# Performance work log

Measured on AMD Instinct MI355X. Metric: run time of the kernel, lower is better.

## Reference

```python
import jax, jax.numpy as jnp
import numpy as np
import math

B, T, C, H = 2, 2048, 1024, 16
HD = C // H
WINDOW = 256  # local_attn_ctx with attnblocksize=1


def setup_inputs() -> dict:
    key = jax.random.key(0)
    k1, k2, k3 = jax.random.split(key, 3)
    x = jax.random.normal(k1, (B, T, C), dtype=jnp.float32)
    Wqkv = jax.random.normal(k2, (C, 3 * C), dtype=jnp.float32) * 0.02
    bqkv = jnp.zeros((3 * C,), dtype=jnp.float32)
    Wproj = jax.random.normal(k3, (C, C), dtype=jnp.float32) * 0.02
    bproj = jnp.zeros((C,), dtype=jnp.float32)
    # 'local' block-sparse layout at token granularity: causal + sliding window
    i = np.arange(T)[:, None]
    j = np.arange(T)[None, :]
    mask = ((j <= i) & (i - j <= WINDOW)).astype(np.int32)
    return {"x": x, "Wqkv": Wqkv, "bqkv": bqkv, "Wproj": Wproj, "bproj": bproj,
            "mask": jnp.asarray(mask)}


def reference(x, Wqkv, bqkv, Wproj, bproj, mask):
    Bb, Tt, Cc = x.shape
    qkv = (x @ Wqkv + bqkv).reshape(Bb, Tt, 3, H, HD)  # [B,T,3,H,hd]
    q = jnp.transpose(qkv[:, :, 0], (0, 2, 1, 3))  # [B,H,T,hd]
    k = jnp.transpose(qkv[:, :, 1], (0, 2, 1, 3))
    v = jnp.transpose(qkv[:, :, 2], (0, 2, 1, 3))
    scale = 1.0 / math.sqrt(HD)
    att = jnp.einsum('bhqd,bhkd->bhqk', q, k) * scale  # dense T x T scores
    att = jnp.where(mask[:Tt, :Tt] == 0, -jnp.inf, att)
    att = jax.nn.softmax(att, axis=-1)
    y = jnp.einsum('bhqk,bhkd->bhqd', att, v)
    y = jnp.transpose(y, (0, 2, 1, 3)).reshape(Bb, Tt, Cc)
    return y @ Wproj + bproj
```

## Files before the change

### kernel.cpp

```cpp
#include <hip/hip_runtime.h>
#include <hip/hip_bf16.h>
#include <math.h>

typedef __bf16 bf16;
typedef __attribute__((ext_vector_type(8))) __bf16 bf16x8;
typedef __attribute__((ext_vector_type(4))) __bf16 bf16x4;
typedef __attribute__((ext_vector_type(4))) float f32x4;

#define B_  2
#define T_  2048
#define C_  1024
#define H_  16
#define HD_ 64
#define WIN_ 256

#define GLOAD16(g, l)                                                        \
  __builtin_amdgcn_global_load_lds(                                          \
      (const __attribute__((address_space(1))) void*)(g),                    \
      (__attribute__((address_space(3))) void*)(l), 16, 0, 0)

__device__ inline void bar() {
  asm volatile("" ::: "memory");
  __builtin_amdgcn_s_barrier();
  asm volatile("" ::: "memory");
}


__global__ __launch_bounds__(256) void prologue_k(const float* __restrict__ x,
                                                  bf16* __restrict__ xb,
                                                  const float* __restrict__ Wqkv,
                                                  bf16* __restrict__ wqkvT,
                                                  const float* __restrict__ Wproj,
                                                  bf16* __restrict__ wprojT) {
  __shared__ float t[32][33];
  const int blk = blockIdx.x;
  const int tid = threadIdx.x;

  if (blk < 4096) {
    const int idx = blk * 256 + tid;
    const float4 v = ((const float4*)x)[idx];
    bf16x4 o;
    o[0] = (bf16)v.x; o[1] = (bf16)v.y; o[2] = (bf16)v.z; o[3] = (bf16)v.w;
    ((bf16x4*)xb)[idx] = o;
    return;
  }

  const float* W; bf16* WT; int N, tb;
  if (blk < 4096 + 3072) { tb = blk - 4096; W = Wqkv;  WT = wqkvT;  N = 3 * C_; }
  else                   { tb = blk - 7168; W = Wproj; WT = wprojT; N = C_;     }
  const int xt = N / 32;
  const int n0 = (tb % xt) * 32, k0 = (tb / xt) * 32;
  const int tx = tid & 31, ty = tid >> 5;

  #pragma unroll
  for (int i = 0; i < 32; i += 8)
    t[ty + i][tx] = W[(size_t)(k0 + ty + i) * N + (n0 + tx)];
  __syncthreads();
  #pragma unroll
  for (int i = 0; i < 32; i += 8)
    WT[(size_t)(n0 + ty + i) * C_ + (k0 + tx)] = (bf16)t[tx][ty + i];
}


template <int TM, int TN, int WM, int WN, int MINW, int MODE>
__global__ __launch_bounds__(WM * WN * 64, MINW)
void gemm_db_k(const bf16* __restrict__ A, const bf16* __restrict__ Bt,
               const float* __restrict__ bias,
               void* __restrict__ out0, void* __restrict__ out1,
               int M, int N, int K) {
  constexpr int NW    = WM * WN;
  constexpr int WROWS = TM / WM;
  constexpr int WCOLS = TN / WN;
  constexpr int FM    = WROWS / 16;
  constexpr int FN    = WCOLS / 16;
  constexpr int NCH   = (TM + TN) / 8;
  constexpr int CPW   = NCH / NW;

  const int bm = blockIdx.x * TM;
  const int bn = blockIdx.y * TN;
  const int tid  = threadIdx.x;
  const int wid  = tid >> 6;
  const int lane = tid & 63;
  const int wr = wid / WN;
  const int wc = wid % WN;
  const int lr = lane & 15;
  const int g  = lane >> 4;

  __shared__ bf16 As[2][TM * 64];
  __shared__ bf16 Bs[2][TN * 64];

  f32x4 acc[FM][FN] = {};

  const int sr = lane >> 3;
  const int sc = ((lane & 7) ^ sr) << 3;

  #define STG(p_, u_)                                                        \
    do {                                                                     \
      _Pragma("unroll")                                                      \
      for (int i = 0; i < CPW; ++i) {                                        \
        const int c = wid * CPW + i;                                         \
        if (c < TM / 8) {                                                    \
          GLOAD16(A + (size_t)(bm + c * 8 + sr) * K + (u_) * 64 + sc,        \
                  &As[p_][c * 8 * 64]);                                      \
        } else {                                                             \
          GLOAD16(Bt + (size_t)(bn + (c - TM / 8) * 8 + sr) * K + (u_) * 64 + sc, \
                  &Bs[p_][(c - TM / 8) * 8 * 64]);                           \
        }                                                                    \
      }                                                                      \
    } while (0)

  const int NT = K >> 6;
  const int kc0 = ((0 + g) ^ (lr & 7)) << 3;
  const int kc1 = ((4 + g) ^ (lr & 7)) << 3;

  STG(0, 0);
  asm volatile("s_waitcnt vmcnt(0)" ::: "memory");
  __builtin_amdgcn_s_barrier();
  asm volatile("" ::: "memory");

  for (int u = 0; u < NT; ++u) {
    const int p = u & 1;
    if (u + 1 < NT) {
      STG(p ^ 1, u + 1);
      asm volatile("s_waitcnt vmcnt(%0)" :: "i"(CPW) : "memory");
    } else {
      asm volatile("s_waitcnt vmcnt(0)" ::: "memory");
    }
    bar();

    const bf16* Ar = &As[p][(wr * WROWS + lr) * 64];
    const bf16* Br = &Bs[p][(wc * WCOLS + lr) * 64];
    #pragma unroll
    for (int s = 0; s < 2; ++s) {
      const int kc = s ? kc1 : kc0;
      bf16x8 av[FM], bvv[FN];
      #pragma unroll
      for (int m = 0; m < FM; ++m)
        av[m] = *(const bf16x8*)(Ar + m * 16 * 64 + kc);
      #pragma unroll
      for (int n = 0; n < FN; ++n)
        bvv[n] = *(const bf16x8*)(Br + n * 16 * 64 + kc);
      __builtin_amdgcn_s_setprio(1);
      #pragma unroll
      for (int m = 0; m < FM; ++m)
        #pragma unroll
        for (int n = 0; n < FN; ++n)
          acc[m][n] = __builtin_amdgcn_mfma_f32_16x16x32_bf16(av[m], bvv[n], acc[m][n], 0, 0, 0);
      __builtin_amdgcn_s_setprio(0);
    }
    bar();
  }
  #undef STG

  const int orow = g * 4;
  #pragma unroll
  for (int n = 0; n < FN; ++n) {
    const int nbase = bn + wc * WCOLS + n * 16;
    const int gn = nbase + lr;
    const float bv_ = bias[gn];
    #pragma unroll
    for (int m = 0; m < FM; ++m) {
      const int gm0 = bm + wr * WROWS + m * 16 + orow;
      if (MODE == 0) {
        #pragma unroll
        for (int r = 0; r < 4; ++r)
          ((float*)out0)[(size_t)(gm0 + r) * N + gn] = acc[m][n][r] + bv_;
      } else {
        if (nbase < 2 * C_) {
          #pragma unroll
          for (int r = 0; r < 4; ++r)
            ((bf16*)out0)[(size_t)(gm0 + r) * (2 * C_) + gn] = (bf16)(acc[m][n][r] + bv_);
        } else {
          const int vcol = gn - 2 * C_;
          const int h = vcol >> 6, d = vcol & 63;
          const int b = gm0 >> 11, tok = gm0 & (T_ - 1);
          bf16x4 o;
          #pragma unroll
          for (int r = 0; r < 4; ++r) o[r] = (bf16)(acc[m][n][r] + bv_);
          *(bf16x4*)&((bf16*)out1)[(((size_t)b * H_ + h) * HD_ + d) * T_ + tok] = o;
        }
      }
    }
  }
}


__global__ __launch_bounds__(512) void attn_mfma2_k(const bf16* __restrict__ qk,
                                                    const bf16* __restrict__ vt,
                                                    bf16* __restrict__ y) {
  const int q0 = blockIdx.x * 128;
  const int h  = blockIdx.y;
  const int b  = blockIdx.z;
  const int tid  = threadIdx.x;
  const int wid  = tid >> 6;
  const int lane = tid & 63;
  const int lr = lane & 15;
  const int g  = lane >> 4;

  __shared__ bf16 Ks[2][64 * 64];
  __shared__ bf16 Vs[2][64 * 64];
  __shared__ bf16 Ps[8][16][72];

  const int qrow = q0 + wid * 16 + lr;
  const bf16* qptr = qk + ((size_t)(b * T_ + qrow)) * (2 * C_) + h * HD_;
  bf16x8 qf0 = *(const bf16x8*)(qptr + g * 8);
  bf16x8 qf1 = *(const bf16x8*)(qptr + 32 + g * 8);

  float m = -1e30f, l = 0.f;
  f32x4 yacc[4] = {};

  const int bx = blockIdx.x;
  const int kt_lo = (bx * 2 >= 4) ? bx * 2 - 4 : 0;
  const int kt_hi = bx * 2 + 1;

  const int sr = lane >> 3;
  const int sc = ((lane & 7) ^ sr) << 3;
  const int kc0 = ((0 + g) ^ (lr & 7)) << 3;
  const int kc1 = ((4 + g) ^ (lr & 7)) << 3;

  #define STAGEKV(p_, kt_)                                                     \
    do {                                                                       \
      _Pragma("unroll")                                                        \
      for (int i = 0; i < 2; ++i) {                                            \
        const int c = wid * 2 + i;                                             \
        if (c < 8)                                                             \
          GLOAD16(qk + ((size_t)(b * T_) + (kt_) * 64 + c * 8 + sr) * (2 * C_) \
                       + C_ + h * HD_ + sc,                                    \
                  &Ks[p_][c * 8 * 64]);                                        \
        else                                                                   \
          GLOAD16(vt + (((size_t)b * H_ + h) * HD_ + (c - 8) * 8 + sr) * T_    \
                       + (kt_) * 64 + sc,                                      \
                  &Vs[p_][(c - 8) * 8 * 64]);                                  \
      }                                                                        \
    } while (0)

  STAGEKV(0, kt_lo);
  asm volatile("s_waitcnt vmcnt(0)" ::: "memory");
  bar();

  for (int kt = kt_lo; kt <= kt_hi; ++kt) {
    const int idx = kt - kt_lo;
    const int p   = idx & 1;
    if (kt + 1 <= kt_hi) {
      STAGEKV(p ^ 1, kt + 1);
      asm volatile("s_waitcnt vmcnt(2)" ::: "memory");
    } else {
      asm volatile("s_waitcnt vmcnt(0)" ::: "memory");
    }
    bar();

    const int wq = q0 + wid * 16;
    if (kt * 64 <= wq + 15 && kt * 64 + 63 >= wq - WIN_) {
      f32x4 sacc[4] = {};
      __builtin_amdgcn_s_setprio(1);
      #pragma unroll
      for (int t = 0; t < 4; ++t) {
        sacc[t] = __builtin_amdgcn_mfma_f32_16x16x32_bf16(
            *(const bf16x8*)&Ks[p][(t * 16 + lr) * 64 + kc0], qf0, sacc[t], 0, 0, 0);
        sacc[t] = __builtin_amdgcn_mfma_f32_16x16x32_bf16(
            *(const bf16x8*)&Ks[p][(t * 16 + lr) * 64 + kc1], qf1, sacc[t], 0, 0, 0);
      }
      __builtin_amdgcn_s_setprio(0);

      float pv[4][4];
      float rmax = -1e30f;
      #pragma unroll
      for (int t = 0; t < 4; ++t)
        #pragma unroll
        for (int r = 0; r < 4; ++r) {
          const int key = kt * 64 + t * 16 + g * 4 + r;
          const bool valid = (key <= qrow) && (qrow - key <= WIN_);
          const float sv = valid ? sacc[t][r] * 0.125f : -__builtin_inff();
          pv[t][r] = sv;
          rmax = fmaxf(rmax, sv);
        }
      rmax = fmaxf(rmax, __shfl_xor(rmax, 16));
      rmax = fmaxf(rmax, __shfl_xor(rmax, 32));

      const float mnew = fmaxf(m, rmax);
      const float alpha = __expf(m - mnew);
      m = mnew;
      float lsum = 0.f;
      #pragma unroll
      for (int t = 0; t < 4; ++t)
        #pragma unroll
        for (int r = 0; r < 4; ++r) {
          const float e = __expf(pv[t][r] - mnew);
          pv[t][r] = e;
          lsum += e;
        }
      lsum += __shfl_xor(lsum, 16);
      lsum += __shfl_xor(lsum, 32);
      l = l * alpha + lsum;

      #pragma unroll
      for (int t = 0; t < 4; ++t) {
        bf16x4 pk;
        #pragma unroll
        for (int r = 0; r < 4; ++r) pk[r] = (bf16)pv[t][r];
        *(bf16x4*)&Ps[wid][lr][t * 16 + g * 4] = pk;
      }

      float al[4];
      #pragma unroll
      for (int r = 0; r < 4; ++r) al[r] = __shfl(alpha, g * 4 + r);
      #pragma unroll
      for (int t = 0; t < 4; ++t)
        #pragma unroll
        for (int r = 0; r < 4; ++r) yacc[t][r] *= al[r];

      bf16x8 pf0 = *(const bf16x8*)&Ps[wid][lr][g * 8];
      bf16x8 pf1 = *(const bf16x8*)&Ps[wid][lr][32 + g * 8];
      __builtin_amdgcn_s_setprio(1);
      #pragma unroll
      for (int t = 0; t < 4; ++t) {
        yacc[t] = __builtin_amdgcn_mfma_f32_16x16x32_bf16(
            pf0, *(const bf16x8*)&Vs[p][(t * 16 + lr) * 64 + kc0], yacc[t], 0, 0, 0);
        yacc[t] = __builtin_amdgcn_mfma_f32_16x16x32_bf16(
            pf1, *(const bf16x8*)&Vs[p][(t * 16 + lr) * 64 + kc1], yacc[t], 0, 0, 0);
      }
      __builtin_amdgcn_s_setprio(0);
    }
    bar();
  }
  #undef STAGEKV

  float li[4];
  #pragma unroll
  for (int r = 0; r < 4; ++r) li[r] = 1.f / __shfl(l, g * 4 + r);
  #pragma unroll
  for (int t = 0; t < 4; ++t)
    #pragma unroll
    for (int r = 0; r < 4; ++r) {
      const int tok = q0 + wid * 16 + g * 4 + r;
      y[((size_t)(b * T_ + tok)) * C_ + h * HD_ + t * 16 + lr] = (bf16)(yacc[t][r] * li[r]);
    }
}


extern "C" void kernel_launch(void* const* d_in, const int* in_sizes, int n_in,
                              void* d_out, int out_size, void* d_ws, size_t ws_size,
                              hipStream_t stream) {
  const float* x     = (const float*)d_in[0];
  const float* Wqkv  = (const float*)d_in[1];
  const float* bqkv  = (const float*)d_in[2];
  const float* Wproj = (const float*)d_in[3];
  const float* bproj = (const float*)d_in[4];
  float* out = (float*)d_out;

  const size_t SZ_QK  = (size_t)B_ * T_ * 2 * C_ * sizeof(bf16);
  const size_t SZ_VT  = (size_t)B_ * H_ * HD_ * T_ * sizeof(bf16);
  const size_t SZ_XB  = (size_t)B_ * T_ * C_ * sizeof(bf16);
  const size_t SZ_WQT = (size_t)3 * C_ * C_ * sizeof(bf16);
  const size_t SZ_WPT = (size_t)C_ * C_ * sizeof(bf16);
  const size_t NEED   = SZ_QK + SZ_VT + SZ_XB + SZ_WQT + SZ_WPT + SZ_XB;
  if (ws_size < NEED) return;

  char* ws = (char*)d_ws;
  bf16* qkb    = (bf16*)(ws);
  bf16* vtb    = (bf16*)(ws + SZ_QK);
  bf16* xb     = (bf16*)(ws + SZ_QK + SZ_VT);
  bf16* wqkvT  = (bf16*)(ws + SZ_QK + SZ_VT + SZ_XB);
  bf16* wprojT = (bf16*)(ws + SZ_QK + SZ_VT + SZ_XB + SZ_WQT);
  bf16* yb     = (bf16*)(ws + SZ_QK + SZ_VT + SZ_XB + SZ_WQT + SZ_WPT);

  prologue_k<<<8192, 256, 0, stream>>>(x, xb, Wqkv, wqkvT, Wproj, wprojT);

  gemm_db_k<64, 96, 2, 2, 4, 2><<<dim3((B_ * T_) / 64, (3 * C_) / 96), 256, 0, stream>>>(
      xb, wqkvT, bqkv, qkb, vtb, B_ * T_, 3 * C_, C_);

  attn_mfma2_k<<<dim3(T_ / 128, H_, B_), 512, 0, stream>>>(qkb, vtb, yb);

  gemm_db_k<64, 128, 2, 2, 2, 0><<<dim3((B_ * T_) / 64, C_ / 128), 256, 0, stream>>>(
      yb, wprojT, bproj, out, nullptr, B_ * T_, C_, C_);
}
```

Baseline: 89.22 us.

## Fuse all stages into one cooperative persistent kernel with grid syncs

Replaces the four separate launches (prologue, QKV GEMM, attention, projection GEMM) with a single cooperative kernel of 512 blocks of 512 threads. A grid-wide sync separates the phases, and shared memory is reused from one pool. The QKV GEMM tile grows to 128x192 with 8 warps, the prologue is re-mapped to 512 blocks, and there is a multi-launch fallback if the cooperative launch fails. This removes launch gaps and tail effects between kernels, at the cost of grid-sync overhead, occupancy limits from a 80KB LDS pool, and fewer blocks per phase.

```diff
diff --git a/kernel.cpp b/kernel.cpp
--- a/kernel.cpp
+++ b/kernel.cpp
@@ -1,6 +1,9 @@
 #include <hip/hip_runtime.h>
+#include <hip/hip_cooperative_groups.h>
 #include <hip/hip_bf16.h>
 #include <math.h>
+
+namespace cg = cooperative_groups;
 
 typedef __bf16 bf16;
 typedef __attribute__((ext_vector_type(8))) __bf16 bf16x8;
@@ -26,48 +29,52 @@
 }
 
 
-__global__ __launch_bounds__(256) void prologue_k(const float* __restrict__ x,
-                                                  bf16* __restrict__ xb,
-                                                  const float* __restrict__ Wqkv,
-                                                  bf16* __restrict__ wqkvT,
-                                                  const float* __restrict__ Wproj,
-                                                  bf16* __restrict__ wprojT) {
-  __shared__ float t[32][33];
-  const int blk = blockIdx.x;
+__device__ __forceinline__ void prologue_phase(const float* __restrict__ x,
+                                               bf16* __restrict__ xb,
+                                               const float* __restrict__ Wqkv,
+                                               bf16* __restrict__ wqkvT,
+                                               const float* __restrict__ Wproj,
+                                               bf16* __restrict__ wprojT,
+                                               float* tf, int bid) {
   const int tid = threadIdx.x;
-
-  if (blk < 4096) {
-    const int idx = blk * 256 + tid;
+  #pragma unroll
+  for (int i = 0; i < 4; ++i) {
+    const int idx = (bid * 512 + tid) + i * 262144;
     const float4 v = ((const float4*)x)[idx];
     bf16x4 o;
     o[0] = (bf16)v.x; o[1] = (bf16)v.y; o[2] = (bf16)v.z; o[3] = (bf16)v.w;
     ((bf16x4*)xb)[idx] = o;
-    return;
-  }
-
-  const float* W; bf16* WT; int N, tb;
-  if (blk < 4096 + 3072) { tb = blk - 4096; W = Wqkv;  WT = wqkvT;  N = 3 * C_; }
-  else                   { tb = blk - 7168; W = Wproj; WT = wprojT; N = C_;     }
-  const int xt = N / 32;
-  const int n0 = (tb % xt) * 32, k0 = (tb / xt) * 32;
-  const int tx = tid & 31, ty = tid >> 5;
-
-  #pragma unroll
-  for (int i = 0; i < 32; i += 8)
-    t[ty + i][tx] = W[(size_t)(k0 + ty + i) * N + (n0 + tx)];
-  __syncthreads();
-  #pragma unroll
-  for (int i = 0; i < 32; i += 8)
-    WT[(size_t)(n0 + ty + i) * C_ + (k0 + tx)] = (bf16)t[tx][ty + i];
-}
-
-
-template <int TM, int TN, int WM, int WN, int MINW, int MODE>
-__global__ __launch_bounds__(WM * WN * 64, MINW)
-void gemm_db_k(const bf16* __restrict__ A, const bf16* __restrict__ Bt,
-               const float* __restrict__ bias,
-               void* __restrict__ out0, void* __restrict__ out1,
-               int M, int N, int K) {
+  }
+  const int half = tid >> 8;
+  const int st = tid & 255;
+  const int tx = st & 31, ty = st >> 5;
+  float* tt = tf + half * (32 * 33);
+  for (int j = 0; j < 4; ++j) {
+    const int tile = bid * 8 + j * 2 + half;
+    const float* W; bf16* WT; int N, tb;
+    if (tile < 3072) { tb = tile;        W = Wqkv;  WT = wqkvT;  N = 3 * C_; }
+    else             { tb = tile - 3072; W = Wproj; WT = wprojT; N = C_;     }
+    const int xt = N / 32;
+    const int n0 = (tb % xt) * 32, k0 = (tb / xt) * 32;
+    #pragma unroll
+    for (int i = 0; i < 32; i += 8)
+      tt[(ty + i) * 33 + tx] = W[(size_t)(k0 + ty + i) * N + (n0 + tx)];
+    __syncthreads();
+    #pragma unroll
+    for (int i = 0; i < 32; i += 8)
+      WT[(size_t)(n0 + ty + i) * C_ + (k0 + tx)] = (bf16)tt[tx * 33 + (ty + i)];
+    __syncthreads();
+  }
+}
+
+template <int TM, int TN, int WM, int WN, int MODE>
+__device__ __forceinline__ void gemm_phase(const bf16* __restrict__ A,
+                                           const bf16* __restrict__ Bt,
+                                           const float* __restrict__ bias,
+                                           void* __restrict__ out0,
+                                           void* __restrict__ out1,
+                                           int M, int N, int K,
+                                           bf16* pool, int bx, int by) {
   constexpr int NW    = WM * WN;
   constexpr int WROWS = TM / WM;
   constexpr int WCOLS = TN / WN;
@@ -76,8 +83,11 @@
   constexpr int NCH   = (TM + TN) / 8;
   constexpr int CPW   = NCH / NW;
 
-  const int bm = blockIdx.x * TM;
-  const int bn = blockIdx.y * TN;
+  bf16* As = pool;
+  bf16* Bs = pool + 2 * TM * 64;
+
+  const int bm = bx * TM;
+  const int bn = by * TN;
   const int tid  = threadIdx.x;
   const int wid  = tid >> 6;
   const int lane = tid & 63;
@@ -86,25 +96,22 @@
   const int lr = lane & 15;
   const int g  = lane >> 4;
 
-  __shared__ bf16 As[2][TM * 64];
-  __shared__ bf16 Bs[2][TN * 64];
-
   f32x4 acc[FM][FN] = {};
 
   const int sr = lane >> 3;
   const int sc = ((lane & 7) ^ sr) << 3;
 
-  #define STG(p_, u_)                                                        \
+  #define STGF(p_, u_)                                                       \
     do {                                                                     \
       _Pragma("unroll")                                                      \
       for (int i = 0; i < CPW; ++i) {                                        \
         const int c = wid * CPW + i;                                         \
         if (c < TM / 8) {                                                    \
           GLOAD16(A + (size_t)(bm + c * 8 + sr) * K + (u_) * 64 + sc,        \
-                  &As[p_][c * 8 * 64]);                                      \
+                  As + (p_) * TM * 64 + c * 8 * 64);                         \
         } else {                                                             \
           GLOAD16(Bt + (size_t)(bn + (c - TM / 8) * 8 + sr) * K + (u_) * 64 + sc, \
-                  &Bs[p_][(c - TM / 8) * 8 * 64]);                           \
+                  Bs + (p_) * TN * 64 + (c - TM / 8) * 8 * 64);              \
         }                                                                    \
       }                                                                      \
     } while (0)
@@ -113,7 +120,7 @@
   const int kc0 = ((0 + g) ^ (lr & 7)) << 3;
   const int kc1 = ((4 + g) ^ (lr & 7)) << 3;
 
-  STG(0, 0);
+  STGF(0, 0);
   asm volatile("s_waitcnt vmcnt(0)" ::: "memory");
   __builtin_amdgcn_s_barrier();
   asm volatile("" ::: "memory");
@@ -121,15 +128,15 @@
   for (int u = 0; u < NT; ++u) {
     const int p = u & 1;
     if (u + 1 < NT) {
-      STG(p ^ 1, u + 1);
+      STGF(p ^ 1, u + 1);
       asm volatile("s_waitcnt vmcnt(%0)" :: "i"(CPW) : "memory");
     } else {
       asm volatile("s_waitcnt vmcnt(0)" ::: "memory");
     }
     bar();
 
-    const bf16* Ar = &As[p][(wr * WROWS + lr) * 64];
-    const bf16* Br = &Bs[p][(wc * WCOLS + lr) * 64];
+    const bf16* Ar = As + p * TM * 64 + (wr * WROWS + lr) * 64;
+    const bf16* Br = Bs + p * TN * 64 + (wc * WCOLS + lr) * 64;
     #pragma unroll
     for (int s = 0; s < 2; ++s) {
       const int kc = s ? kc1 : kc0;
@@ -150,7 +157,7 @@
     }
     bar();
   }
-  #undef STG
+  #undef STGF
 
   const int orow = g * 4;
   #pragma unroll
@@ -184,23 +191,21 @@
   }
 }
 
-
-__global__ __launch_bounds__(512) void attn_mfma2_k(const bf16* __restrict__ qk,
-                                                    const bf16* __restrict__ vt,
-                                                    bf16* __restrict__ y) {
-  const int q0 = blockIdx.x * 128;
-  const int h  = blockIdx.y;
-  const int b  = blockIdx.z;
+__device__ __forceinline__ void attn_phase(const bf16* __restrict__ qk,
+                                           const bf16* __restrict__ vt,
+                                           bf16* __restrict__ y,
+                                           bf16* pool, int bx, int h, int b) {
+  bf16* Ks = pool;
+  bf16* Vs = pool + 8192;
+  bf16* Ps = pool + 16384;
+
+  const int q0 = bx * 128;
   const int tid  = threadIdx.x;
   const int wid  = tid >> 6;
   const int lane = tid & 63;
   const int lr = lane & 15;
   const int g  = lane >> 4;
 
-  __shared__ bf16 Ks[2][64 * 64];
-  __shared__ bf16 Vs[2][64 * 64];
-  __shared__ bf16 Ps[8][16][72];
-
   const int qrow = q0 + wid * 16 + lr;
   const bf16* qptr = qk + ((size_t)(b * T_ + qrow)) * (2 * C_) + h * HD_;
   bf16x8 qf0 = *(const bf16x8*)(qptr + g * 8);
@@ -209,7 +214,6 @@
   float m = -1e30f, l = 0.f;
   f32x4 yacc[4] = {};
 
-  const int bx = blockIdx.x;
   const int kt_lo = (bx * 2 >= 4) ? bx * 2 - 4 : 0;
   const int kt_hi = bx * 2 + 1;
 
@@ -226,11 +230,11 @@
         if (c < 8)                                                             \
           GLOAD16(qk + ((size_t)(b * T_) + (kt_) * 64 + c * 8 + sr) * (2 * C_) \
                        + C_ + h * HD_ + sc,                                    \
-                  &Ks[p_][c * 8 * 64]);                                        \
+                  Ks + (p_) * 4096 + c * 8 * 64);                              \
         else                                                                   \
           GLOAD16(vt + (((size_t)b * H_ + h) * HD_ + (c - 8) * 8 + sr) * T_    \
                        + (kt_) * 64 + sc,                                      \
-                  &Vs[p_][(c - 8) * 8 * 64]);                                  \
+                  Vs + (p_) * 4096 + (c - 8) * 8 * 64);                        \
       }                                                                        \
     } while (0)
 
@@ -256,9 +260,9 @@
       #pragma unroll
       for (int t = 0; t < 4; ++t) {
         sacc[t] = __builtin_amdgcn_mfma_f32_16x16x32_bf16(
-            *(const bf16x8*)&Ks[p][(t * 16 + lr) * 64 + kc0], qf0, sacc[t], 0, 0, 0);
+            *(const bf16x8*)(Ks + p * 4096 + (t * 16 + lr) * 64 + kc0), qf0, sacc[t], 0, 0, 0);
         sacc[t] = __builtin_amdgcn_mfma_f32_16x16x32_bf16(
-            *(const bf16x8*)&Ks[p][(t * 16 + lr) * 64 + kc1], qf1, sacc[t], 0, 0, 0);
+            *(const bf16x8*)(Ks + p * 4096 + (t * 16 + lr) * 64 + kc1), qf1, sacc[t], 0, 0, 0);
       }
       __builtin_amdgcn_s_setprio(0);
 
@@ -298,7 +302,7 @@
         bf16x4 pk;
         #pragma unroll
         for (int r = 0; r < 4; ++r) pk[r] = (bf16)pv[t][r];
-        *(bf16x4*)&Ps[wid][lr][t * 16 + g * 4] = pk;
+        *(bf16x4*)(Ps + (wid * 16 + lr) * 72 + t * 16 + g * 4) = pk;
       }
 
       float al[4];
@@ -309,15 +313,15 @@
         #pragma unroll
         for (int r = 0; r < 4; ++r) yacc[t][r] *= al[r];
 
-      bf16x8 pf0 = *(const bf16x8*)&Ps[wid][lr][g * 8];
-      bf16x8 pf1 = *(const bf16x8*)&Ps[wid][lr][32 + g * 8];
+      bf16x8 pf0 = *(const bf16x8*)(Ps + (wid * 16 + lr) * 72 + g * 8);
+      bf16x8 pf1 = *(const bf16x8*)(Ps + (wid * 16 + lr) * 72 + 32 + g * 8);
       __builtin_amdgcn_s_setprio(1);
       #pragma unroll
       for (int t = 0; t < 4; ++t) {
         yacc[t] = __builtin_amdgcn_mfma_f32_16x16x32_bf16(
-            pf0, *(const bf16x8*)&Vs[p][(t * 16 + lr) * 64 + kc0], yacc[t], 0, 0, 0);
+            pf0, *(const bf16x8*)(Vs + p * 4096 + (t * 16 + lr) * 64 + kc0), yacc[t], 0, 0, 0);
         yacc[t] = __builtin_amdgcn_mfma_f32_16x16x32_bf16(
-            pf1, *(const bf16x8*)&Vs[p][(t * 16 + lr) * 64 + kc1], yacc[t], 0, 0, 0);
+            pf1, *(const bf16x8*)(Vs + p * 4096 + (t * 16 + lr) * 64 + kc1), yacc[t], 0, 0, 0);
       }
       __builtin_amdgcn_s_setprio(0);
     }
@@ -338,6 +342,55 @@
 }
 
 
+__global__ __launch_bounds__(512, 4) void fused_k(
+    const float* __restrict__ x, bf16* __restrict__ xb,
+    const float* __restrict__ Wqkv, bf16* __restrict__ wqkvT,
+    const float* __restrict__ Wproj, bf16* __restrict__ wprojT,
+    const float* __restrict__ bqkv, const float* __restrict__ bproj,
+    bf16* __restrict__ qkb, bf16* __restrict__ vtb,
+    bf16* __restrict__ yb, float* __restrict__ out) {
+  __shared__ __align__(16) bf16 pool[40960];
+  cg::grid_group grid = cg::this_grid();
+  const int bid = blockIdx.x;
+
+  prologue_phase(x, xb, Wqkv, wqkvT, Wproj, wprojT, (float*)pool, bid);
+  grid.sync();
+  gemm_phase<128, 192, 2, 4, 2>(xb, wqkvT, bqkv, qkb, vtb,
+                                B_ * T_, 3 * C_, C_, pool, bid & 31, bid >> 5);
+  grid.sync();
+  attn_phase(qkb, vtb, yb, pool, bid & 15, (bid >> 4) & 15, bid >> 8);
+  grid.sync();
+  gemm_phase<64, 128, 2, 4, 0>(yb, wprojT, bproj, out, nullptr,
+                               B_ * T_, C_, C_, pool, bid & 63, bid >> 6);
+}
+
+
+__global__ __launch_bounds__(512) void prologue_k(const float* x, bf16* xb,
+    const float* Wqkv, bf16* wqkvT, const float* Wproj, bf16* wprojT) {
+  __shared__ __align__(16) float tf[2 * 32 * 33];
+  prologue_phase(x, xb, Wqkv, wqkvT, Wproj, wprojT, tf, blockIdx.x);
+}
+
+__global__ __launch_bounds__(512, 4) void qkv_k(const bf16* A, const bf16* Bt,
+    const float* bias, void* out0, void* out1) {
+  __shared__ __align__(16) bf16 pool[40960];
+  gemm_phase<128, 192, 2, 4, 2>(A, Bt, bias, out0, out1,
+                                B_ * T_, 3 * C_, C_, pool, blockIdx.x, blockIdx.y);
+}
+
+__global__ __launch_bounds__(512) void attn_k(const bf16* qk, const bf16* vt, bf16* y) {
+  __shared__ __align__(16) bf16 pool[25600];
+  attn_phase(qk, vt, y, pool, blockIdx.x, blockIdx.y, blockIdx.z);
+}
+
+__global__ __launch_bounds__(512, 4) void proj_k(const bf16* A, const bf16* Bt,
+    const float* bias, void* out0) {
+  __shared__ __align__(16) bf16 pool[24576];
+  gemm_phase<64, 128, 2, 4, 0>(A, Bt, bias, out0, nullptr,
+                               B_ * T_, C_, C_, pool, blockIdx.x, blockIdx.y);
+}
+
+
 extern "C" void kernel_launch(void* const* d_in, const int* in_sizes, int n_in,
                               void* d_out, int out_size, void* d_ws, size_t ws_size,
                               hipStream_t stream) {
@@ -364,13 +417,15 @@
   bf16* wprojT = (bf16*)(ws + SZ_QK + SZ_VT + SZ_XB + SZ_WQT);
   bf16* yb     = (bf16*)(ws + SZ_QK + SZ_VT + SZ_XB + SZ_WQT + SZ_WPT);
 
-  prologue_k<<<8192, 256, 0, stream>>>(x, xb, Wqkv, wqkvT, Wproj, wprojT);
-
-  gemm_db_k<64, 96, 2, 2, 4, 2><<<dim3((B_ * T_) / 64, (3 * C_) / 96), 256, 0, stream>>>(
-      xb, wqkvT, bqkv, qkb, vtb, B_ * T_, 3 * C_, C_);
-
-  attn_mfma2_k<<<dim3(T_ / 128, H_, B_), 512, 0, stream>>>(qkb, vtb, yb);
-
-  gemm_db_k<64, 128, 2, 2, 2, 0><<<dim3((B_ * T_) / 64, C_ / 128), 256, 0, stream>>>(
-      yb, wprojT, bproj, out, nullptr, B_ * T_, C_, C_);
-}
+  void* args[] = {(void*)&x, (void*)&xb, (void*)&Wqkv, (void*)&wqkvT,
+                  (void*)&Wproj, (void*)&wprojT, (void*)&bqkv, (void*)&bproj,
+                  (void*)&qkb, (void*)&vtb, (void*)&yb, (void*)&out};
+  hipError_t err = hipLaunchCooperativeKernel((void*)fused_k, dim3(512), dim3(512),
+                                              args, 0, stream);
+  if (err != hipSuccess) {
+    prologue_k<<<512, 512, 0, stream>>>(x, xb, Wqkv, wqkvT, Wproj, wprojT);
+    qkv_k<<<dim3(32, 16), 512, 0, stream>>>(xb, wqkvT, bqkv, qkb, vtb);
+    attn_k<<<dim3(16, 16, 2), 512, 0, stream>>>(qkb, vtb, yb);
+    proj_k<<<dim3(64, 8), 512, 0, stream>>>(yb, wprojT, bproj, out);
+  }
+}
```

Result: slower. 276.3 us (+209.6%).
